# Kernel tuning notes

Hardware: AMD Instinct MI355X
Metric: run time of the kernel (lower is better)

## Reference

```python
import jax, jax.numpy as jnp
import numpy as np

TEMPERATURE = 0.07
EPS = 1e-12  # F.normalize eps


def _l2_normalize(x):
    # matches torch F.normalize(dim=1): x / max(||x||, eps)
    n = jnp.linalg.norm(x, axis=1, keepdims=True)
    return x / jnp.maximum(n, EPS)


def setup_inputs() -> dict:
    key = jax.random.key(0)
    k1, k2 = jax.random.split(key)
    N, Z = 4096, 256
    z1 = jax.random.normal(k1, (N, Z), dtype=jnp.float32)
    z2 = jax.random.normal(k2, (N, Z), dtype=jnp.float32)
    return {"z1": z1, "z2": z2}


def reference(z1, z2):
    N = z1.shape[0]
    z1n = _l2_normalize(z1)
    z2n = _l2_normalize(z2)
    reps = jnp.concatenate([z1n, z2n], axis=0)          # [2N, Z]
    sim = reps @ reps.T                                  # cosine sim (rows unit-norm)
    # positives: sim[i, i+N] for i<N and sim[i, i-N] for i>=N
    pos = jnp.concatenate([jnp.diagonal(sim, offset=N),
                           jnp.diagonal(sim, offset=-N)])  # [2N]
    # The row logits are {positive} U {all sims except self and positive},
    # i.e. all entries except the self-similarity diagonal.
    inv_t = 1.0 / TEMPERATURE
    twoN = 2 * N
    diag_mask = jnp.eye(twoN, dtype=bool)
    logits = jnp.where(diag_mask, -jnp.inf, sim * inv_t)   # [2N, 2N]
    lse = jax.nn.logsumexp(logits, axis=1)                 # [2N]
    # cross_entropy with label at the positive: -pos/T + lse, sum / 2N
    loss = jnp.mean(lse - pos * inv_t)
    return loss
```

## Files before the change

kernel.cpp:

```cpp
#include <hip/hip_runtime.h>
#include <hip/hip_bf16.h>

#define N_ROWS 4096
#define TWO_N  8192
#define ZDIM   256
#define INV_T  (1.0f/0.07f)
#define EXP_SCALE (INV_T * 1.44269504088896340736f)

typedef __attribute__((ext_vector_type(8))) short bf16x8;
typedef __attribute__((ext_vector_type(4))) float f32x4;

__device__ __forceinline__ void async_load16(const void* g, void* lds_uniform_base) {
  __builtin_amdgcn_global_load_lds(
      (const __attribute__((address_space(1))) void*)g,
      (__attribute__((address_space(3))) void*)lds_uniform_base, 16, 0, 0);
}

__global__ __launch_bounds__(256) void normalize_kernel(
    const float* __restrict__ z1, const float* __restrict__ z2,
    __hip_bfloat16* __restrict__ reps, float* __restrict__ pos,
    float* __restrict__ out) {
  const int b = blockIdx.x;
  const int t = threadIdx.x;
  const float x1 = z1[b * ZDIM + t];
  const float x2 = z2[b * ZDIM + t];
  float s1 = x1 * x1, s2 = x2 * x2, s3 = x1 * x2;
  #pragma unroll
  for (int m = 1; m < 64; m <<= 1) {
    s1 += __shfl_xor(s1, m, 64);
    s2 += __shfl_xor(s2, m, 64);
    s3 += __shfl_xor(s3, m, 64);
  }
  __shared__ float red[3][4];
  const int w = t >> 6, l = t & 63;
  if (l == 0) { red[0][w] = s1; red[1][w] = s2; red[2][w] = s3; }
  __syncthreads();
  const float n1 = red[0][0] + red[0][1] + red[0][2] + red[0][3];
  const float n2 = red[1][0] + red[1][1] + red[1][2] + red[1][3];
  const float dt = red[2][0] + red[2][1] + red[2][2] + red[2][3];
  const float inv1 = 1.0f / fmaxf(sqrtf(n1), 1e-12f);
  const float inv2 = 1.0f / fmaxf(sqrtf(n2), 1e-12f);
  reps[b * ZDIM + t]            = __float2bfloat16(x1 * inv1);
  reps[(b + N_ROWS) * ZDIM + t] = __float2bfloat16(x2 * inv2);
  if (t == 0) {
    pos[b] = dt * inv1 * inv2;
    if (b == 0) out[0] = INV_T;
  }
}

__global__ __launch_bounds__(256, 1) void simsum_kernel(
    const __hip_bfloat16* __restrict__ reps,
    float* __restrict__ rowscratch,
    float* __restrict__ colscratch) {
  __shared__ __align__(16) __hip_bfloat16 Alds[128 * 256];
  __shared__ __align__(16) __hip_bfloat16 Blds[128 * 256];
  __shared__ float colred[2][256];

  const int tid  = threadIdx.x;
  const int lane = tid & 63;
  const int wave = tid >> 6;
  const int wm = wave >> 1, wn = wave & 1;
  const int quad = lane >> 4;
  const int l16  = lane & 15;
  const int itile = blockIdx.x;
  const int chunk = blockIdx.y;
  const int rowBase = itile * 128;
  const char* gbase = (const char*)reps;

  #pragma unroll
  for (int p = 0; p < 16; ++p) {
    const int cbase = p * 256 + (wave << 6);
    const int c = cbase + lane;
    const int row = c >> 5;
    const int ch = (c & 31) ^ (row & 7);
    async_load16(gbase + ((rowBase + row) * ZDIM + ch * 8) * 2,
                 (char*)Alds + cbase * 16);
  }
  __syncthreads();

  const int nd = (chunk == 0) ? ((itile < 32) ? 9 : 8) : 8;

  float rowpart[16];
  #pragma unroll
  for (int i = 0; i < 16; ++i) rowpart[i] = 0.0f;

  const f32x4 zero4 = {0.0f, 0.0f, 0.0f, 0.0f};

  for (int td = 0; td < nd; ++td) {
    const int d = (chunk == 0) ? ((td == 8) ? 32 : td) : (chunk * 8 + td);
    const int jtile = (itile + d) & 63;
    const int colBase = jtile * 128;
    const bool diag = (d == 0);

    if (!diag) {
      __syncthreads();
      #pragma unroll
      for (int p = 0; p < 16; ++p) {
        const int cbase = p * 256 + (wave << 6);
        const int c = cbase + lane;
        const int row = c >> 5;
        const int ch = (c & 31) ^ (row & 7);
        async_load16(gbase + ((colBase + row) * ZDIM + ch * 8) * 2,
                     (char*)Blds + cbase * 16);
      }
      __syncthreads();
    }

    f32x4 acc[4][4];
    #pragma unroll
    for (int mi = 0; mi < 4; ++mi)
      #pragma unroll
      for (int ni = 0; ni < 4; ++ni) acc[mi][ni] = zero4;

    #pragma unroll
    for (int kc = 0; kc < 4; ++kc) {
      #pragma unroll
      for (int kk2 = 0; kk2 < 2; ++kk2) {
        const int CH = kc * 8 + kk2 * 4 + quad;
        bf16x8 afrag[4], bfrag[4];
        #pragma unroll
        for (int mi = 0; mi < 4; ++mi) {
          const int m = wm * 64 + mi * 16 + l16;
          afrag[mi] = *(const bf16x8*)((const char*)Alds + (m * 32 + (CH ^ (m & 7))) * 16);
        }
        #pragma unroll
        for (int ni = 0; ni < 4; ++ni) {
          const int n = wn * 64 + ni * 16 + l16;
          const char* src = diag ? (const char*)Alds : (const char*)Blds;
          bfrag[ni] = *(const bf16x8*)(src + (n * 32 + (CH ^ (n & 7))) * 16);
        }
        #pragma unroll
        for (int mi = 0; mi < 4; ++mi)
          #pragma unroll
          for (int ni = 0; ni < 4; ++ni)
            acc[mi][ni] = __builtin_amdgcn_mfma_f32_16x16x32_bf16(
                afrag[mi], bfrag[ni], acc[mi][ni], 0, 0, 0);
      }
    }

    float colpart[4] = {0.0f, 0.0f, 0.0f, 0.0f};
    #pragma unroll
    for (int mi = 0; mi < 4; ++mi) {
      #pragma unroll
      for (int r = 0; r < 4; ++r) {
        const int grow = rowBase + wm * 64 + mi * 16 + quad * 4 + r;
        float s = 0.0f;
        #pragma unroll
        for (int ni = 0; ni < 4; ++ni) {
          const int gcol = colBase + wn * 64 + ni * 16 + l16;
          const float v = acc[mi][ni][r];
          const float e = exp2f((v - 1.0f) * EXP_SCALE);
          if (!diag || grow != gcol) s += e;
          colpart[ni] += e;
        }
        rowpart[mi * 4 + r] += s;
      }
    }
    if (!diag) {
      #pragma unroll
      for (int ni = 0; ni < 4; ++ni) {
        float v = colpart[ni];
        v += __shfl_xor(v, 16, 64);
        v += __shfl_xor(v, 32, 64);
        if (quad == 0) colred[td & 1][wm * 128 + wn * 64 + ni * 16 + l16] = v;
      }
      __syncthreads();
      if (tid < 128)
        colscratch[(jtile * 32 + (d - 1)) * 128 + tid] =
            colred[td & 1][tid] + colred[td & 1][128 + tid];
    }
  }

  #pragma unroll
  for (int i = 0; i < 16; ++i) {
    float v = rowpart[i];
    v += __shfl_xor(v, 1, 64);
    v += __shfl_xor(v, 2, 64);
    v += __shfl_xor(v, 4, 64);
    v += __shfl_xor(v, 8, 64);
    rowpart[i] = v;
  }
  __syncthreads();
  if (l16 == 0) {
    #pragma unroll
    for (int mi = 0; mi < 4; ++mi)
      #pragma unroll
      for (int r = 0; r < 4; ++r)
        colred[0][wn * 128 + wm * 64 + mi * 16 + quad * 4 + r] = rowpart[mi * 4 + r];
  }
  __syncthreads();
  if (tid < 128)
    rowscratch[(itile * 4 + chunk) * 128 + tid] = colred[0][tid] + colred[0][128 + tid];
}

__global__ __launch_bounds__(256) void reduce_kernel(
    const float* __restrict__ rowscratch, const float* __restrict__ colscratch,
    const float* __restrict__ pos, float* __restrict__ out) {
  const int j = blockIdx.x;
  const int tid = threadIdx.x;
  float v = 0.0f;
  if (tid < 128) {
    float s = 0.0f;
    #pragma unroll
    for (int c = 0; c < 4; ++c) s += rowscratch[(j * 4 + c) * 128 + tid];
    const int ns = (j < 32) ? 31 : 32;
    for (int si = 0; si < ns; ++si) s += colscratch[(j * 32 + si) * 128 + tid];
    v = logf(s) * (1.0f / (float)TWO_N);
  } else if (tid < 192) {
    v = -pos[j * 64 + (tid - 128)] * (INV_T / (float)N_ROWS);
  }
  #pragma unroll
  for (int m = 1; m < 64; m <<= 1) v += __shfl_xor(v, m, 64);
  __shared__ float red[4];
  if ((tid & 63) == 0) red[tid >> 6] = v;
  __syncthreads();
  if (tid == 0) atomicAdd(out, red[0] + red[1] + red[2] + red[3]);
}

extern "C" void kernel_launch(void* const* d_in, const int* in_sizes, int n_in,
                              void* d_out, int out_size, void* d_ws, size_t ws_size,
                              hipStream_t stream) {
  const float* z1 = (const float*)d_in[0];
  const float* z2 = (const float*)d_in[1];
  char* ws = (char*)d_ws;
  __hip_bfloat16* reps = (__hip_bfloat16*)ws;
  size_t off = (size_t)TWO_N * ZDIM * 2;
  float* pos = (float*)(ws + off);        off += N_ROWS * 4;
  float* rowscratch = (float*)(ws + off); off += 64 * 4 * 128 * 4;
  float* colscratch = (float*)(ws + off); off += 64 * 32 * 128 * 4;

  normalize_kernel<<<N_ROWS, 256, 0, stream>>>(z1, z2, reps, pos, (float*)d_out);
  simsum_kernel<<<dim3(64, 4), 256, 0, stream>>>(reps, rowscratch, colscratch);
  reduce_kernel<<<64, 256, 0, stream>>>(rowscratch, colscratch, pos, (float*)d_out);
}
```

Before: 113.4 us.

## Switch similarity GEMM to FP8 e4m3 MFMA with halved LDS tiles and doubled grid

The normalized representations are now quantized to FP8 e4m3 with a hand-written converter, and the tile GEMM uses the fp8 16x16x32 MFMA instead of bf16. Tiles take half the bytes, so two blocks can share a CU (launch bounds raised to 2). The grid doubles to 8 chunks, each covering 4 diagonals instead of 8, and the row scratch grows to match. The aim is to cut LDS/global traffic and raise MFMA throughput and occupancy, at the cost of lower-precision cosine similarities. Because the logits are scaled by 1/0.07 before exponentiation, this precision loss may affect the loss accuracy.

After: 100.5 us. -11.3%, faster.

```diff
diff --git a/kernel.cpp b/kernel.cpp
--- a/kernel.cpp
+++ b/kernel.cpp
@@ -7,7 +7,6 @@
 #define INV_T  (1.0f/0.07f)
 #define EXP_SCALE (INV_T * 1.44269504088896340736f)
 
-typedef __attribute__((ext_vector_type(8))) short bf16x8;
 typedef __attribute__((ext_vector_type(4))) float f32x4;
 
 __device__ __forceinline__ void async_load16(const void* g, void* lds_uniform_base) {
@@ -16,9 +15,27 @@
       (__attribute__((address_space(3))) void*)lds_uniform_base, 16, 0, 0);
 }
 
+__device__ __forceinline__ unsigned char f32_to_e4m3(float x) {
+  unsigned int u = __float_as_uint(x);
+  const unsigned int s = u >> 31;
+  unsigned int a = u & 0x7FFFFFFFu;
+  if (a > 0x43E00000u) a = 0x43E00000u;
+  const float f = __uint_as_float(a);
+  unsigned int out;
+  if (a < (121u << 23)) {
+    const int m = (int)rintf(f * 512.0f);
+    out = (unsigned int)m;
+  } else {
+    const unsigned int r = a + 0x7FFFFu + ((a >> 20) & 1u);
+    const unsigned int e8 = (r >> 23) - 120u;
+    out = (e8 << 3) | ((r >> 20) & 7u);
+  }
+  return (unsigned char)(out | (s << 7));
+}
+
 __global__ __launch_bounds__(256) void normalize_kernel(
     const float* __restrict__ z1, const float* __restrict__ z2,
-    __hip_bfloat16* __restrict__ reps, float* __restrict__ pos,
+    unsigned char* __restrict__ reps, float* __restrict__ pos,
     float* __restrict__ out) {
   const int b = blockIdx.x;
   const int t = threadIdx.x;
@@ -40,20 +57,20 @@
   const float dt = red[2][0] + red[2][1] + red[2][2] + red[2][3];
   const float inv1 = 1.0f / fmaxf(sqrtf(n1), 1e-12f);
   const float inv2 = 1.0f / fmaxf(sqrtf(n2), 1e-12f);
-  reps[b * ZDIM + t]            = __float2bfloat16(x1 * inv1);
-  reps[(b + N_ROWS) * ZDIM + t] = __float2bfloat16(x2 * inv2);
+  reps[b * ZDIM + t]            = f32_to_e4m3(x1 * inv1);
+  reps[(b + N_ROWS) * ZDIM + t] = f32_to_e4m3(x2 * inv2);
   if (t == 0) {
     pos[b] = dt * inv1 * inv2;
     if (b == 0) out[0] = INV_T;
   }
 }
 
-__global__ __launch_bounds__(256, 1) void simsum_kernel(
-    const __hip_bfloat16* __restrict__ reps,
+__global__ __launch_bounds__(256, 2) void simsum_kernel(
+    const unsigned char* __restrict__ reps,
     float* __restrict__ rowscratch,
     float* __restrict__ colscratch) {
-  __shared__ __align__(16) __hip_bfloat16 Alds[128 * 256];
-  __shared__ __align__(16) __hip_bfloat16 Blds[128 * 256];
+  __shared__ __align__(16) unsigned char Alds[128 * 256];
+  __shared__ __align__(16) unsigned char Blds[128 * 256];
   __shared__ float colred[2][256];
 
   const int tid  = threadIdx.x;
@@ -68,17 +85,16 @@
   const char* gbase = (const char*)reps;
 
   #pragma unroll
-  for (int p = 0; p < 16; ++p) {
-    const int cbase = p * 256 + (wave << 6);
-    const int c = cbase + lane;
-    const int row = c >> 5;
-    const int ch = (c & 31) ^ (row & 7);
-    async_load16(gbase + ((rowBase + row) * ZDIM + ch * 8) * 2,
-                 (char*)Alds + cbase * 16);
-  }
-  __syncthreads();
-
-  const int nd = (chunk == 0) ? ((itile < 32) ? 9 : 8) : 8;
+  for (int p = 0; p < 8; ++p) {
+    const int c = p * 256 + (wave << 6) + lane;
+    const int row = c >> 4, k16 = c & 15;
+    const int src = (k16 & 8) | ((k16 ^ row) & 7);
+    async_load16(gbase + (rowBase + row) * ZDIM + src * 16,
+                 (char*)Alds + (size_t)c * 16 - (size_t)lane * 16 + (size_t)lane * 16);
+  }
+  __syncthreads();
+
+  const int nd = (chunk == 0) ? ((itile < 32) ? 5 : 4) : 4;
 
   float rowpart[16];
   #pragma unroll
@@ -87,7 +103,7 @@
   const f32x4 zero4 = {0.0f, 0.0f, 0.0f, 0.0f};
 
   for (int td = 0; td < nd; ++td) {
-    const int d = (chunk == 0) ? ((td == 8) ? 32 : td) : (chunk * 8 + td);
+    const int d = (chunk == 0) ? ((td == 4) ? 32 : td) : (chunk * 4 + td);
     const int jtile = (itile + d) & 63;
     const int colBase = jtile * 128;
     const bool diag = (d == 0);
@@ -95,13 +111,11 @@
     if (!diag) {
       __syncthreads();
       #pragma unroll
-      for (int p = 0; p < 16; ++p) {
-        const int cbase = p * 256 + (wave << 6);
-        const int c = cbase + lane;
-        const int row = c >> 5;
-        const int ch = (c & 31) ^ (row & 7);
-        async_load16(gbase + ((colBase + row) * ZDIM + ch * 8) * 2,
-                     (char*)Blds + cbase * 16);
+      for (int p = 0; p < 8; ++p) {
+        const int c = p * 256 + (wave << 6) + lane;
+        const int row = c >> 4, k16 = c & 15;
+        const int src = (k16 & 8) | ((k16 ^ row) & 7);
+        async_load16(gbase + (colBase + row) * ZDIM + src * 16, (char*)Blds + c * 16);
       }
       __syncthreads();
     }
@@ -117,23 +131,26 @@
       #pragma unroll
       for (int kk2 = 0; kk2 < 2; ++kk2) {
         const int CH = kc * 8 + kk2 * 4 + quad;
-        bf16x8 afrag[4], bfrag[4];
+        const int k16 = CH >> 1, half = (CH & 1) * 8;
+        long afrag[4], bfrag[4];
         #pragma unroll
         for (int mi = 0; mi < 4; ++mi) {
           const int m = wm * 64 + mi * 16 + l16;
-          afrag[mi] = *(const bf16x8*)((const char*)Alds + (m * 32 + (CH ^ (m & 7))) * 16);
+          const int sw = (k16 & 8) | ((k16 ^ m) & 7);
+          afrag[mi] = *(const long*)((const char*)Alds + m * 256 + sw * 16 + half);
         }
         #pragma unroll
         for (int ni = 0; ni < 4; ++ni) {
           const int n = wn * 64 + ni * 16 + l16;
+          const int sw = (k16 & 8) | ((k16 ^ n) & 7);
           const char* src = diag ? (const char*)Alds : (const char*)Blds;
-          bfrag[ni] = *(const bf16x8*)(src + (n * 32 + (CH ^ (n & 7))) * 16);
+          bfrag[ni] = *(const long*)(src + n * 256 + sw * 16 + half);
         }
         #pragma unroll
         for (int mi = 0; mi < 4; ++mi)
           #pragma unroll
           for (int ni = 0; ni < 4; ++ni)
-            acc[mi][ni] = __builtin_amdgcn_mfma_f32_16x16x32_bf16(
+            acc[mi][ni] = __builtin_amdgcn_mfma_f32_16x16x32_fp8_fp8(
                 afrag[mi], bfrag[ni], acc[mi][ni], 0, 0, 0);
       }
     }
@@ -190,7 +207,7 @@
   }
   __syncthreads();
   if (tid < 128)
-    rowscratch[(itile * 4 + chunk) * 128 + tid] = colred[0][tid] + colred[0][128 + tid];
+    rowscratch[(itile * 8 + chunk) * 128 + tid] = colred[0][tid] + colred[0][128 + tid];
 }
 
 __global__ __launch_bounds__(256) void reduce_kernel(
@@ -202,7 +219,7 @@
   if (tid < 128) {
     float s = 0.0f;
     #pragma unroll
-    for (int c = 0; c < 4; ++c) s += rowscratch[(j * 4 + c) * 128 + tid];
+    for (int c = 0; c < 8; ++c) s += rowscratch[(j * 8 + c) * 128 + tid];
     const int ns = (j < 32) ? 31 : 32;
     for (int si = 0; si < ns; ++si) s += colscratch[(j * 32 + si) * 128 + tid];
     v = logf(s) * (1.0f / (float)TWO_N);
@@ -223,13 +240,13 @@
   const float* z1 = (const float*)d_in[0];
   const float* z2 = (const float*)d_in[1];
   char* ws = (char*)d_ws;
-  __hip_bfloat16* reps = (__hip_bfloat16*)ws;
-  size_t off = (size_t)TWO_N * ZDIM * 2;
+  unsigned char* reps = (unsigned char*)ws;
+  size_t off = (size_t)TWO_N * ZDIM;
   float* pos = (float*)(ws + off);        off += N_ROWS * 4;
-  float* rowscratch = (float*)(ws + off); off += 64 * 4 * 128 * 4;
+  float* rowscratch = (float*)(ws + off); off += 64 * 8 * 128 * 4;
   float* colscratch = (float*)(ws + off); off += 64 * 32 * 128 * 4;
 
   normalize_kernel<<<N_ROWS, 256, 0, stream>>>(z1, z2, reps, pos, (float*)d_out);
-  simsum_kernel<<<dim3(64, 4), 256, 0, stream>>>(reps, rowscratch, colscratch);
+  simsum_kernel<<<dim3(64, 8), 256, 0, stream>>>(reps, rowscratch, colscratch);
   reduce_kernel<<<64, 256, 0, stream>>>(rowscratch, colscratch, pos, (float*)d_out);
 }
```
